# Performance work log

Measured on AMD Instinct MI355X. Metric: run time of the kernel, lower is better.

The kernel has to match this reference:

```python
import jax, jax.numpy as jnp
import numpy as np

BN_EPS = 1e-5


def _conv_bn_elu(x, w, b, bn_scale, bn_bias, bn_mean, bn_var):
    # 1x1 conv == channel-mixing matmul: x [B,C,H,W], w [O,C]
    y = jnp.einsum('bchw,oc->bohw', x, w) + b[None, :, None, None]
    inv = bn_scale * jax.lax.rsqrt(bn_var + BN_EPS)
    y = y * inv[None, :, None, None] + (bn_bias - bn_mean * inv)[None, :, None, None]
    return jax.nn.elu(y)


def setup_inputs() -> dict:
    key = jax.random.key(0)
    ks = jax.random.split(key, 24)
    B, C, H, W = 4, 128, 64, 64
    d = {}
    d['x_q'] = jax.random.normal(ks[0], (B, C, H, W), jnp.float32)
    d['x_k'] = jax.random.normal(ks[1], (B, C, H, W), jnp.float32)
    d['x_v'] = jax.random.normal(ks[2], (B, C, H, W), jnp.float32)
    scale = 1.0 / np.sqrt(C)
    i = 3
    for p in ('q', 'k', 'v'):
        d[f'{p}_w'] = jax.random.normal(ks[i], (C, C), jnp.float32) * scale; i += 1
        d[f'{p}_b'] = jax.random.normal(ks[i], (C,), jnp.float32) * 0.01; i += 1
        d[f'{p}_bn_scale'] = jnp.ones((C,), jnp.float32) + 0.1 * jax.random.normal(ks[i], (C,), jnp.float32); i += 1
        d[f'{p}_bn_bias'] = 0.1 * jax.random.normal(ks[i], (C,), jnp.float32); i += 1
        d[f'{p}_bn_mean'] = 0.1 * jax.random.normal(ks[i], (C,), jnp.float32); i += 1
        d[f'{p}_bn_var'] = jax.random.uniform(ks[i], (C,), jnp.float32, 0.5, 1.5); i += 1
    # torch inits gamma/beta to zero; use small nonzero values so output is informative
    d['gamma'] = jnp.array([0.5], jnp.float32)
    d['beta'] = jnp.array([0.5], jnp.float32)
    return d


def reference(x_q, x_k, x_v,
              q_w, q_b, q_bn_scale, q_bn_bias, q_bn_mean, q_bn_var,
              k_w, k_b, k_bn_scale, k_bn_bias, k_bn_mean, k_bn_var,
              v_w, v_b, v_bn_scale, v_bn_bias, v_bn_mean, v_bn_var,
              gamma, beta):
    B, C, Hv, Wv = x_v.shape
    q = _conv_bn_elu(x_q, q_w, q_b, q_bn_scale, q_bn_bias, q_bn_mean, q_bn_var).reshape(B, C, -1)  # [B,C,HWq]
    k = _conv_bn_elu(x_k, k_w, k_b, k_bn_scale, k_bn_bias, k_bn_mean, k_bn_var).reshape(B, C, -1)  # [B,C,HWk]
    v = _conv_bn_elu(x_v, v_w, v_b, v_bn_scale, v_bn_bias, v_bn_mean, v_bn_var).reshape(B, C, -1)  # [B,C,HWv]
    energy = jnp.einsum('bcq,bck->bqk', q, k)                 # [B,HWq,HWk] (no scaling, as in source)
    attention = jax.nn.softmax(energy, axis=-1)
    out = jnp.einsum('bck,bqk->bcq', v, attention)            # [B,C,HWq]
    out = out.reshape(B, C, Hv, Wv)
    return gamma * out + beta * x_v
```

## Files before the change

### kernel.cpp

```cpp
#include <hip/hip_runtime.h>

#define CC 128
#define SS 4096
#define L2E 1.44269504f

typedef _Float16 f16;
typedef f16 f16x8 __attribute__((ext_vector_type(8)));
typedef __fp16 h16x2 __attribute__((ext_vector_type(2)));
typedef float f32x4 __attribute__((ext_vector_type(4)));

struct PArg { const float *x, *w, *b, *sc, *bb, *bm, *bv; f16* out; };

__global__ __launch_bounds__(256) void projk(PArg A0, PArg A1, PArg A2) {
    const int p = blockIdx.y;
    PArg A = (p == 0) ? A0 : ((p == 1) ? A1 : A2);
    const int bx = blockIdx.x;
    const int b  = bx >> 6;
    const int s0 = (bx & 63) * 64;
    const int tid = threadIdx.x;
    const int w = tid >> 6, lane = tid & 63;
    const int n = lane & 15, g = lane >> 4;

    __shared__ f16 Xl[64][136];
    __shared__ f16 Wl[128][136];
    f16* Yl = &Wl[0][0];

#pragma unroll
    for (int i = 0; i < 8; ++i) {
        int vi = tid + i * 256;
        int c = vi >> 4, sq = (vi & 15) * 4;
        float4 v = *(const float4*)(A.x + ((size_t)b * CC + c) * SS + s0 + sq);
        Xl[sq + 0][c] = (f16)v.x; Xl[sq + 1][c] = (f16)v.y;
        Xl[sq + 2][c] = (f16)v.z; Xl[sq + 3][c] = (f16)v.w;
    }
#pragma unroll
    for (int i = 0; i < 8; ++i) {
        int vi = tid + i * 256;
        int o = vi >> 4, cq = (vi & 15) * 8;
        float iv = A.sc[o] * rsqrtf(A.bv[o] + 1e-5f);
        const float* wp = A.w + o * CC + cq;
        float4 a = *(const float4*)wp;
        float4 b4 = *(const float4*)(wp + 4);
        union { f16 h[8]; uint4 u; } pk;
        pk.h[0] = (f16)(a.x * iv);  pk.h[1] = (f16)(a.y * iv);
        pk.h[2] = (f16)(a.z * iv);  pk.h[3] = (f16)(a.w * iv);
        pk.h[4] = (f16)(b4.x * iv); pk.h[5] = (f16)(b4.y * iv);
        pk.h[6] = (f16)(b4.z * iv); pk.h[7] = (f16)(b4.w * iv);
        *(uint4*)&Wl[o][cq] = pk.u;
    }
    __syncthreads();

    if (p < 2) {
        const float qsc = (p == 0) ? L2E : 1.0f;
        f32x4 acc[2][4];
#pragma unroll
        for (int mt = 0; mt < 2; ++mt)
#pragma unroll
            for (int nt = 0; nt < 4; ++nt) acc[mt][nt] = (f32x4){0.f, 0.f, 0.f, 0.f};
#pragma unroll
        for (int ks = 0; ks < 4; ++ks) {
            f16x8 af[2], bf[4];
#pragma unroll
            for (int mt = 0; mt < 2; ++mt) af[mt] = *(const f16x8*)&Wl[w * 32 + mt * 16 + n][ks * 32 + g * 8];
#pragma unroll
            for (int nt = 0; nt < 4; ++nt) bf[nt] = *(const f16x8*)&Xl[nt * 16 + n][ks * 32 + g * 8];
#pragma unroll
            for (int mt = 0; mt < 2; ++mt)
#pragma unroll
                for (int nt = 0; nt < 4; ++nt)
                    acc[mt][nt] = __builtin_amdgcn_mfma_f32_16x16x32_f16(af[mt], bf[nt], acc[mt][nt], 0, 0, 0);
        }
        __syncthreads();
#pragma unroll
        for (int mt = 0; mt < 2; ++mt) {
            float ebr[4];
#pragma unroll
            for (int r = 0; r < 4; ++r) {
                int o = w * 32 + mt * 16 + g * 4 + r;
                float iv = A.sc[o] * rsqrtf(A.bv[o] + 1e-5f);
                ebr[r] = (A.b[o] - A.bm[o]) * iv + A.bb[o];
            }
#pragma unroll
            for (int nt = 0; nt < 4; ++nt) {
                union { f16 h[4]; uint2 u; } pk;
#pragma unroll
                for (int r = 0; r < 4; ++r) {
                    float y = acc[mt][nt][r] + ebr[r];
                    y = (y > 0.f) ? y : (__expf(y) - 1.f);
                    pk.h[r] = (f16)(y * qsc);
                }
                *(uint2*)&Yl[(nt * 16 + n) * 136 + w * 32 + mt * 16 + g * 4] = pk.u;
            }
        }
        __syncthreads();
#pragma unroll
        for (int i = 0; i < 4; ++i) {
            int vi = tid + i * 256;
            int s = vi >> 4, cl = (vi & 15) * 8;
            *(uint4*)&A.out[((size_t)b * SS + s0 + s) * CC + cl] = *(const uint4*)&Yl[s * 136 + cl];
        }
    } else {
        f32x4 acc[8];
#pragma unroll
        for (int nt = 0; nt < 8; ++nt) acc[nt] = (f32x4){0.f, 0.f, 0.f, 0.f};
#pragma unroll
        for (int ks = 0; ks < 4; ++ks) {
            f16x8 af = *(const f16x8*)&Xl[w * 16 + n][ks * 32 + g * 8];
#pragma unroll
            for (int nt = 0; nt < 8; ++nt) {
                f16x8 bf = *(const f16x8*)&Wl[nt * 16 + n][ks * 32 + g * 8];
                acc[nt] = __builtin_amdgcn_mfma_f32_16x16x32_f16(af, bf, acc[nt], 0, 0, 0);
            }
        }
        __syncthreads();
#pragma unroll
        for (int nt = 0; nt < 8; ++nt) {
            int o = nt * 16 + n;
            float iv = A.sc[o] * rsqrtf(A.bv[o] + 1e-5f);
            float ebc = (A.b[o] - A.bm[o]) * iv + A.bb[o];
            union { f16 h[4]; uint2 u; } pk;
#pragma unroll
            for (int r = 0; r < 4; ++r) {
                float y = acc[nt][r] + ebc;
                y = (y > 0.f) ? y : (__expf(y) - 1.f);
                pk.h[r] = (f16)y;
            }
            *(uint2*)&Yl[(nt * 16 + n) * 136 + w * 16 + g * 4] = pk.u;
        }
        __syncthreads();
#pragma unroll
        for (int i = 0; i < 4; ++i) {
            int vi = tid + i * 256;
            int o = vi >> 3, sl = (vi & 7) * 8;
            *(uint4*)&A.out[((size_t)b * CC + o) * SS + s0 + sl] = *(const uint4*)&Yl[o * 136 + sl];
        }
    }
}

__device__ __forceinline__ int vswz(int u) {
    return (u & ~7) | ((u ^ (u >> 3)) & 7);
}

__global__ __launch_bounds__(256, 3) void attnk(
    const f16* __restrict__ Qt, const f16* __restrict__ Kt, const f16* __restrict__ Vt,
    f16* __restrict__ Op, float* __restrict__ Ml)
{
    const int tid = threadIdx.x;
    const int bx = blockIdx.x;
    const int kh = bx & 7;
    const int b  = (bx >> 3) & 3;
    const int qt = bx >> 5;
    const int q0 = qt * 128;
    const int kbeg = kh * 512;

    __shared__ __align__(16) char arena[43008];
    const int w = tid >> 6, lane = tid & 63;
    const int n = lane & 15, g = lane >> 4;
    char* Pb = arena + 32768 + w * 2560;

    f16x8 qf[2][4];
    {
        const f16* Qb = Qt + ((size_t)b * SS + q0 + w * 32) * CC;
#pragma unroll
        for (int qt2 = 0; qt2 < 2; ++qt2)
#pragma unroll
            for (int ks = 0; ks < 4; ++ks)
                qf[qt2][ks] = *(const f16x8*)&Qb[(qt2 * 16 + n) * CC + ks * 32 + g * 8];
    }

    f32x4 oacc[8][2];
#pragma unroll
    for (int mtc = 0; mtc < 8; ++mtc)
#pragma unroll
        for (int qt2 = 0; qt2 < 2; ++qt2) oacc[mtc][qt2] = (f32x4){0.f, 0.f, 0.f, 0.f};
    float mreg[2] = {-1e30f, -1e30f}, lsum[2] = {0.f, 0.f};

    int koff[4];
#pragma unroll
    for (int ks = 0; ks < 4; ++ks)
        koff[ks] = n * 256 + (((ks * 4 + g) ^ (n & 7)) << 4);
    int voff[8];
#pragma unroll
    for (int mtc = 0; mtc < 8; ++mtc)
        voff[mtc] = vswz((mtc * 16 + n) * 4 + g) << 4;
    const int rk0 = tid >> 4, c16k = tid & 15;
    const int kst0 = rk0 * 256 + ((c16k ^ (rk0 & 7)) << 4);
    const int rv0 = tid >> 2, cvg = tid & 3;
    const int vw0 = vswz(tid) << 4, vw1 = vswz(tid + 256) << 4;

    {
        char* Kb = arena;
        char* Vb = arena + 16384;
        const f16* Ksrc = Kt + ((size_t)b * SS + kbeg) * CC;
        const f16* Vsrc = Vt + (size_t)b * CC * SS + kbeg;
        *(uint4*)(Kb + kst0)        = *(const uint4*)&Ksrc[rk0 * CC + c16k * 8];
        *(uint4*)(Kb + kst0 + 4096) = *(const uint4*)&Ksrc[(rk0 + 16) * CC + c16k * 8];
        *(uint4*)(Vb + vw0) = *(const uint4*)&Vsrc[(size_t)rv0 * SS + cvg * 8];
        *(uint4*)(Vb + vw1) = *(const uint4*)&Vsrc[(size_t)(rv0 + 64) * SS + cvg * 8];
    }

    for (int kt = 0; kt < 16; ++kt) {
        const int cur = kt & 1;
        char* Kb = arena + cur * 8192;
        char* Vb = arena + 16384 + cur * 8192;
        char* Kn = arena + (1 - cur) * 8192;
        char* Vn = arena + 16384 + (1 - cur) * 8192;

        __syncthreads();

        uint4 nk0, nk1, nv0, nv1;
        if (kt < 15) {
            const int k1 = kbeg + (kt + 1) * 32;
            const f16* Ksrc = Kt + ((size_t)b * SS + k1) * CC;
            const f16* Vsrc = Vt + (size_t)b * CC * SS + k1;
            nk0 = *(const uint4*)&Ksrc[rk0 * CC + c16k * 8];
            nk1 = *(const uint4*)&Ksrc[(rk0 + 16) * CC + c16k * 8];
            nv0 = *(const uint4*)&Vsrc[(size_t)rv0 * SS + cvg * 8];
            nv1 = *(const uint4*)&Vsrc[(size_t)(rv0 + 64) * SS + cvg * 8];
        }

        f32x4 sacc[2][2];
#pragma unroll
        for (int kt2 = 0; kt2 < 2; ++kt2)
#pragma unroll
            for (int qt2 = 0; qt2 < 2; ++qt2) sacc[kt2][qt2] = (f32x4){0.f, 0.f, 0.f, 0.f};
        __builtin_amdgcn_s_setprio(1);
#pragma unroll
        for (int ks = 0; ks < 4; ++ks) {
            f16x8 kf[2];
            kf[0] = *(const f16x8*)(Kb + koff[ks]);
            kf[1] = *(const f16x8*)(Kb + koff[ks] + 4096);
#pragma unroll
            for (int kt2 = 0; kt2 < 2; ++kt2)
#pragma unroll
                for (int qt2 = 0; qt2 < 2; ++qt2)
                    sacc[kt2][qt2] = __builtin_amdgcn_mfma_f32_16x16x32_f16(kf[kt2], qf[qt2][ks], sacc[kt2][qt2], 0, 0, 0);
        }
        __builtin_amdgcn_s_setprio(0);

        if (kt < 15) {
            *(uint4*)(Kn + kst0)        = nk0;
            *(uint4*)(Kn + kst0 + 4096) = nk1;
            *(uint4*)(Vn + vw0) = nv0;
            *(uint4*)(Vn + vw1) = nv1;
        }

        float pmax[2];
#pragma unroll
        for (int qt2 = 0; qt2 < 2; ++qt2) {
            float v = fmaxf(fmaxf(fmaxf(sacc[0][qt2][0], sacc[0][qt2][1]),
                                  fmaxf(sacc[0][qt2][2], sacc[0][qt2][3])),
                            fmaxf(fmaxf(sacc[1][qt2][0], sacc[1][qt2][1]),
                                  fmaxf(sacc[1][qt2][2], sacc[1][qt2][3])));
            v = fmaxf(v, __shfl_xor(v, 16));
            v = fmaxf(v, __shfl_xor(v, 32));
            pmax[qt2] = v;
        }
        if (!__all((pmax[0] <= mreg[0] + 12.f) && (pmax[1] <= mreg[1] + 12.f))) {
#pragma unroll
            for (int qt2 = 0; qt2 < 2; ++qt2) {
                float mn = fmaxf(mreg[qt2], pmax[qt2]);
                float al = exp2f(mreg[qt2] - mn);
                mreg[qt2] = mn;
                lsum[qt2] *= al;
#pragma unroll
                for (int mtc = 0; mtc < 8; ++mtc) oacc[mtc][qt2] *= al;
            }
        }
#pragma unroll
        for (int qt2 = 0; qt2 < 2; ++qt2) {
            const float mn = mreg[qt2];
            float rs = 0.f;
#pragma unroll
            for (int kt2 = 0; kt2 < 2; ++kt2) {
                float p0 = exp2f(sacc[kt2][qt2][0] - mn);
                float p1 = exp2f(sacc[kt2][qt2][1] - mn);
                float p2 = exp2f(sacc[kt2][qt2][2] - mn);
                float p3 = exp2f(sacc[kt2][qt2][3] - mn);
                rs += (p0 + p1) + (p2 + p3);
                union { h16x2 h[2]; uint2 u; } pk;
                pk.h[0] = __builtin_amdgcn_cvt_pkrtz(p0, p1);
                pk.h[1] = __builtin_amdgcn_cvt_pkrtz(p2, p3);
                *(uint2*)(Pb + (qt2 * 16 + n) * 80 + kt2 * 32 + g * 8) = pk.u;
            }
            lsum[qt2] += rs;
        }

        {
            f16x8 pf[2];
            pf[0] = *(const f16x8*)(Pb + n * 80 + g * 16);
            pf[1] = *(const f16x8*)(Pb + (16 + n) * 80 + g * 16);
            __builtin_amdgcn_s_setprio(1);
#pragma unroll
            for (int mtc = 0; mtc < 8; ++mtc) {
                f16x8 vf = *(const f16x8*)(Vb + voff[mtc]);
#pragma unroll
                for (int qt2 = 0; qt2 < 2; ++qt2)
                    oacc[mtc][qt2] = __builtin_amdgcn_mfma_f32_16x16x32_f16(vf, pf[qt2], oacc[mtc][qt2], 0, 0, 0);
            }
            __builtin_amdgcn_s_setprio(0);
        }
    }

    float lreg[2];
#pragma unroll
    for (int qt2 = 0; qt2 < 2; ++qt2) {
        float s = lsum[qt2];
        s += __shfl_xor(s, 16);
        s += __shfl_xor(s, 32);
        lreg[qt2] = s;
    }

    const int pidx = (b * 32 + qt) * 8 + kh;
    if (g == 0) {
        float* MlW = Ml + (size_t)pidx * 256;
#pragma unroll
        for (int qt2 = 0; qt2 < 2; ++qt2) {
            int q = w * 32 + qt2 * 16 + n;
            MlW[q]       = mreg[qt2];
            MlW[128 + q] = lreg[qt2];
        }
    }

    __syncthreads();
    f16 (*S2)[136] = (f16(*)[136])arena;
#pragma unroll
    for (int mtc = 0; mtc < 8; ++mtc)
#pragma unroll
        for (int qt2 = 0; qt2 < 2; ++qt2)
#pragma unroll
            for (int r = 0; r < 4; ++r)
                S2[mtc * 16 + g * 4 + r][w * 32 + qt2 * 16 + n] = (f16)oacc[mtc][qt2][r];
    __syncthreads();
    f16* OpW = Op + (size_t)pidx * 16384;
#pragma unroll
    for (int i = 0; i < 8; ++i) {
        int vi = tid + i * 256;
        int c = vi >> 4, qq = (vi & 15) * 8;
        *(uint4*)&OpW[c * 128 + qq] = *(const uint4*)&S2[c][qq];
    }
}

__global__ __launch_bounds__(256) void mrgk(
    const f16* __restrict__ Op, const float* __restrict__ Ml,
    const float* __restrict__ xv, const float* __restrict__ gp, const float* __restrict__ bp,
    float* __restrict__ out)
{
    const int bx = blockIdx.x;
    const int cg = bx & 3, bqt = bx >> 2;
    const int b = bqt >> 5, qt = bqt & 31;
    const int tid = threadIdx.x;
    const int q = tid & 127, hf = tid >> 7;

    const float* ml = Ml + (size_t)bqt * 8 * 256;
    float m = -1e30f;
#pragma unroll
    for (int k2 = 0; k2 < 8; ++k2) m = fmaxf(m, ml[k2 * 256 + q]);
    float wt[8], tot = 0.f;
#pragma unroll
    for (int k2 = 0; k2 < 8; ++k2) {
        wt[k2] = exp2f(ml[k2 * 256 + q] - m);
        tot += wt[k2] * ml[k2 * 256 + 128 + q];
    }
    float inv = 1.f / tot;
    float gm = gp[0], bb = bp[0];

    const f16* O = Op + (size_t)bqt * 8 * 16384;
#pragma unroll 2
    for (int i = 0; i < 16; ++i) {
        int c = cg * 32 + hf * 16 + i;
        float o = 0.f;
#pragma unroll
        for (int k2 = 0; k2 < 8; ++k2) o += wt[k2] * (float)O[k2 * 16384 + c * 128 + q];
        o *= inv;
        size_t idx = ((size_t)(b * CC + c)) * SS + qt * 128 + q;
        out[idx] = gm * o + bb * xv[idx];
    }
}

extern "C" void kernel_launch(void* const* d_in, const int* in_sizes, int n_in,
                              void* d_out, int out_size, void* d_ws, size_t ws_size,
                              hipStream_t stream) {
    (void)in_sizes; (void)n_in; (void)out_size; (void)ws_size;

    const size_t TEN = (size_t)4 * SS * CC;
    f16* Qt = (f16*)d_ws;
    f16* Kt = Qt + TEN;
    f16* Vt = Kt + TEN;
    f16* Op = Vt + TEN;
    float* Ml = (float*)(Op + (size_t)1024 * 16384);

    PArg aq = { (const float*)d_in[0], (const float*)d_in[3],  (const float*)d_in[4],
                (const float*)d_in[5], (const float*)d_in[6],  (const float*)d_in[7],
                (const float*)d_in[8],  Qt };
    PArg ak = { (const float*)d_in[1], (const float*)d_in[9],  (const float*)d_in[10],
                (const float*)d_in[11], (const float*)d_in[12], (const float*)d_in[13],
                (const float*)d_in[14], Kt };
    PArg av = { (const float*)d_in[2], (const float*)d_in[15], (const float*)d_in[16],
                (const float*)d_in[17], (const float*)d_in[18], (const float*)d_in[19],
                (const float*)d_in[20], Vt };

    hipLaunchKernelGGL(projk, dim3(256, 3), dim3(256), 0, stream, aq, ak, av);
    hipLaunchKernelGGL(attnk, dim3(1024), dim3(256), 0, stream, Qt, Kt, Vt, Op, Ml);
    hipLaunchKernelGGL(mrgk, dim3(512), dim3(256), 0, stream,
                       Op, Ml, (const float*)d_in[2], (const float*)d_in[21],
                       (const float*)d_in[22], (float*)d_out);
}
```

Baseline: 191.0 us.

## Vectorize merge kernel loads and make online softmax rescale unconditional

The merge kernel now computes the per-split softmax weights once into shared memory, with the 1/total normalisation folded in. Each thread then reads 8 contiguous f16 partial outputs per split with 128-bit loads and writes float4 results, replacing scalar 2-byte loads and 4-byte stores. The aim is to cut the number of memory instructions and improve coalescing in the merge pass. In the attention loop, the lazy rescale (taken only when the new max exceeds the old by 12) is replaced by an unconditional rescale every tile, which removes a wave vote and branch but adds 16 vector multiplies plus exp2 per tile.

```diff
diff --git a/kernel.cpp b/kernel.cpp
--- a/kernel.cpp
+++ b/kernel.cpp
@@ -245,7 +245,7 @@
             *(uint4*)(Vn + vw1) = nv1;
         }
 
-        float pmax[2];
+        float al[2];
 #pragma unroll
         for (int qt2 = 0; qt2 < 2; ++qt2) {
             float v = fmaxf(fmaxf(fmaxf(sacc[0][qt2][0], sacc[0][qt2][1]),
@@ -254,22 +254,9 @@
                                   fmaxf(sacc[1][qt2][2], sacc[1][qt2][3])));
             v = fmaxf(v, __shfl_xor(v, 16));
             v = fmaxf(v, __shfl_xor(v, 32));
-            pmax[qt2] = v;
-        }
-        if (!__all((pmax[0] <= mreg[0] + 12.f) && (pmax[1] <= mreg[1] + 12.f))) {
-#pragma unroll
-            for (int qt2 = 0; qt2 < 2; ++qt2) {
-                float mn = fmaxf(mreg[qt2], pmax[qt2]);
-                float al = exp2f(mreg[qt2] - mn);
-                mreg[qt2] = mn;
-                lsum[qt2] *= al;
-#pragma unroll
-                for (int mtc = 0; mtc < 8; ++mtc) oacc[mtc][qt2] *= al;
-            }
-        }
-#pragma unroll
-        for (int qt2 = 0; qt2 < 2; ++qt2) {
-            const float mn = mreg[qt2];
+            float mn = fmaxf(mreg[qt2], v);
+            al[qt2] = exp2f(mreg[qt2] - mn);
+            mreg[qt2] = mn;
             float rs = 0.f;
 #pragma unroll
             for (int kt2 = 0; kt2 < 2; ++kt2) {
@@ -283,8 +270,13 @@
                 pk.h[1] = __builtin_amdgcn_cvt_pkrtz(p2, p3);
                 *(uint2*)(Pb + (qt2 * 16 + n) * 80 + kt2 * 32 + g * 8) = pk.u;
             }
-            lsum[qt2] += rs;
-        }
+            lsum[qt2] = lsum[qt2] * al[qt2] + rs;
+        }
+#pragma unroll
+        for (int mtc = 0; mtc < 8; ++mtc)
+#pragma unroll
+            for (int qt2 = 0; qt2 < 2; ++qt2)
+                oacc[mtc][qt2] *= al[qt2];
 
         {
             f16x8 pf[2];
@@ -350,31 +342,61 @@
     const int cg = bx & 3, bqt = bx >> 2;
     const int b = bqt >> 5, qt = bqt & 31;
     const int tid = threadIdx.x;
-    const int q = tid & 127, hf = tid >> 7;
-
-    const float* ml = Ml + (size_t)bqt * 8 * 256;
-    float m = -1e30f;
-#pragma unroll
-    for (int k2 = 0; k2 < 8; ++k2) m = fmaxf(m, ml[k2 * 256 + q]);
-    float wt[8], tot = 0.f;
-#pragma unroll
-    for (int k2 = 0; k2 < 8; ++k2) {
-        wt[k2] = exp2f(ml[k2 * 256 + q] - m);
-        tot += wt[k2] * ml[k2 * 256 + 128 + q];
-    }
-    float inv = 1.f / tot;
-    float gm = gp[0], bb = bp[0];
-
+
+    __shared__ float winv[8][128];
+
+    if (tid < 128) {
+        const int q = tid;
+        const float* ml = Ml + (size_t)bqt * 8 * 256;
+        float m = -1e30f;
+#pragma unroll
+        for (int k2 = 0; k2 < 8; ++k2) m = fmaxf(m, ml[k2 * 256 + q]);
+        float wt[8], tot = 0.f;
+#pragma unroll
+        for (int k2 = 0; k2 < 8; ++k2) {
+            wt[k2] = exp2f(ml[k2 * 256 + q] - m);
+            tot += wt[k2] * ml[k2 * 256 + 128 + q];
+        }
+        float inv = 1.f / tot;
+#pragma unroll
+        for (int k2 = 0; k2 < 8; ++k2) winv[k2][q] = wt[k2] * inv;
+    }
+    __syncthreads();
+
+    const float gm = gp[0], bb = bp[0];
+    const int cl = tid >> 4, qg = tid & 15;
     const f16* O = Op + (size_t)bqt * 8 * 16384;
-#pragma unroll 2
-    for (int i = 0; i < 16; ++i) {
-        int c = cg * 32 + hf * 16 + i;
-        float o = 0.f;
-#pragma unroll
-        for (int k2 = 0; k2 < 8; ++k2) o += wt[k2] * (float)O[k2 * 16384 + c * 128 + q];
-        o *= inv;
-        size_t idx = ((size_t)(b * CC + c)) * SS + qt * 128 + q;
-        out[idx] = gm * o + bb * xv[idx];
+
+#pragma unroll
+    for (int cp = 0; cp < 2; ++cp) {
+        const int c = cg * 32 + cp * 16 + cl;
+        float acc[8];
+#pragma unroll
+        for (int j = 0; j < 8; ++j) acc[j] = 0.f;
+#pragma unroll
+        for (int k2 = 0; k2 < 8; ++k2) {
+            union { uint4 u; f16 h[8]; } ov;
+            ov.u = *(const uint4*)&O[k2 * 16384 + c * 128 + qg * 8];
+            float4 wa = *(const float4*)&winv[k2][qg * 8];
+            float4 wb = *(const float4*)&winv[k2][qg * 8 + 4];
+            acc[0] += wa.x * (float)ov.h[0];
+            acc[1] += wa.y * (float)ov.h[1];
+            acc[2] += wa.z * (float)ov.h[2];
+            acc[3] += wa.w * (float)ov.h[3];
+            acc[4] += wb.x * (float)ov.h[4];
+            acc[5] += wb.y * (float)ov.h[5];
+            acc[6] += wb.z * (float)ov.h[6];
+            acc[7] += wb.w * (float)ov.h[7];
+        }
+        size_t idx = ((size_t)(b * CC + c)) * SS + qt * 128 + qg * 8;
+        float4 xa = *(const float4*)&xv[idx];
+        float4 xb = *(const float4*)&xv[idx + 4];
+        float4 oa = { gm * acc[0] + bb * xa.x, gm * acc[1] + bb * xa.y,
+                      gm * acc[2] + bb * xa.z, gm * acc[3] + bb * xa.w };
+        float4 ob = { gm * acc[4] + bb * xb.x, gm * acc[5] + bb * xb.y,
+                      gm * acc[6] + bb * xb.z, gm * acc[7] + bb * xb.w };
+        *(float4*)&out[idx]     = oa;
+        *(float4*)&out[idx + 4] = ob;
     }
 }
 
```

New measurement: 193.7 us. No clear change (+1.4%).
